# Optimization experiments

Hardware: AMD Instinct MI355X
Metric: run time of the kernel (lower is better)

## Reference

```python
import jax, jax.numpy as jnp
import numpy as np

N, LC, LQ, D = 16, 2048, 256, 256  # D = 2 * LSTM_HIDDEN_DIM


def setup_inputs() -> dict:
    key = jax.random.key(0)
    k1, k2, k3 = jax.random.split(key, 3)
    emb_context = jax.random.normal(k1, (N, LC, D), dtype=jnp.float32)
    emb_query = jax.random.normal(k2, (N, LQ, D), dtype=jnp.float32)
    # Linear(6H=3D, 1, bias=False) weight, flattened to (3D,)
    W = jax.random.normal(k3, (3 * D,), dtype=jnp.float32) / np.sqrt(3 * D)
    return {"emb_context": emb_context, "emb_query": emb_query, "W": W}


def reference(emb_context, emb_query, W):
    d = emb_context.shape[-1]
    # Algebraic decomposition of the expand+cat+linear similarity score:
    # S[n,i,j] = c_i . w_c + q_j . w_q + sum_d c_i[d]*q_j[d]*w_m[d]
    w_c, w_q, w_m = W[:d], W[d:2 * d], W[2 * d:]
    S = (
        jnp.einsum('ncd,d->nc', emb_context, w_c)[:, :, None]
        + jnp.einsum('nqd,d->nq', emb_query, w_q)[:, None, :]
        + jnp.einsum('ncd,nqd->ncq', emb_context * w_m, emb_query)
    )  # (N, Lc, Lq)
    # context-to-query attention
    c2q_attn = jnp.einsum('ncq,nqd->ncd', jax.nn.softmax(S, axis=-1), emb_query)
    # query-to-context attention (max over query dim, softmax over context dim)
    b = jax.nn.softmax(jnp.max(S, axis=2), axis=-1)  # (N, Lc)
    q2c_attn = jnp.einsum('nc,ncd->nd', b, emb_context)[:, None, :]  # (N, 1, D), broadcasts over Lc
    G = jnp.concatenate(
        [emb_context, c2q_attn, emb_context * c2q_attn, emb_context * q2c_attn],
        axis=2,
    )  # (N, Lc, 4D) == (N, Lc, 8*LSTM_HIDDEN_DIM)
    return G
```

## Files before the change

kernel.cpp:

```cpp
#include <hip/hip_runtime.h>
#include <math.h>

#define BN 16
#define LC 2048
#define LQ 256
#define DD 256
#define BM 128
#define NT 512

typedef _Float16 half8 __attribute__((ext_vector_type(8)));
typedef float f32x16 __attribute__((ext_vector_type(16)));

typedef const __attribute__((address_space(1))) void* gas_p;
typedef __attribute__((address_space(3))) void* lds_p;
#define GLOAD_LDS16(gp, lp) \
    __builtin_amdgcn_global_load_lds((gas_p)(gp), (lds_p)(lp), 16, 0, 0)

__device__ __forceinline__ float waveReduceSum(float v) {
#pragma unroll
    for (int o = 32; o > 0; o >>= 1) v += __shfl_xor(v, o, 64);
    return v;
}
__device__ __forceinline__ float waveReduceMax(float v) {
#pragma unroll
    for (int o = 32; o > 0; o >>= 1) v = fmaxf(v, __shfl_xor(v, o, 64));
    return v;
}

__global__ __launch_bounds__(256) void k_prep(const float* __restrict__ q,
                                              const float* __restrict__ W,
                                              _Float16* __restrict__ Qh,
                                              _Float16* __restrict__ QTh,
                                              float* __restrict__ cq) {
    __shared__ float tile[32][257];
    const int n = blockIdx.y;
    const int q0 = blockIdx.x * 32;
    const int t = threadIdx.x;

#pragma unroll
    for (int i = 0; i < 32; ++i) {
        const float v = q[((size_t)(n * LQ + q0 + i)) * DD + t];
        Qh[((size_t)(n * LQ + q0 + i)) * DD + t] = (_Float16)v;
        tile[i][t] = v;
    }
    __syncthreads();

    {
        const int row = t >> 3, sub = t & 7;
        float s = 0.f;
#pragma unroll
        for (int j = 0; j < 32; ++j)
            s = fmaf(tile[row][sub * 32 + j], W[DD + sub * 32 + j], s);
        s += __shfl_xor(s, 1, 64);
        s += __shfl_xor(s, 2, 64);
        s += __shfl_xor(s, 4, 64);
        if (sub == 0) cq[n * LQ + q0 + row] = s;
    }

    const int tx = t & 31, ty = t >> 5;
#pragma unroll
    for (int db = 0; db < 8; ++db) {
#pragma unroll
        for (int i = 0; i < 4; ++i) {
            const int d = db * 32 + ty + 8 * i;
            QTh[((size_t)(n * DD + d)) * LQ + q0 + tx] = (_Float16)tile[tx][d];
        }
    }
}

__global__ __launch_bounds__(NT) void k_main(const float* __restrict__ ctx,
                                             const _Float16* __restrict__ Qh,
                                             const _Float16* __restrict__ QTh,
                                             const float* __restrict__ cq,
                                             const float* __restrict__ W,
                                             float* __restrict__ out,
                                             float* __restrict__ pq,
                                             float* __restrict__ KS) {
    __shared__ _Float16 Abuf[BM * 256];
    __shared__ _Float16 Bbuf[2][256 * 64];
    __shared__ float rowterm[BM];
    __shared__ float eexp[BM];
    __shared__ float redmax[4][BM];
    __shared__ float redsum[4][BM];

    const int t = threadIdx.x;
    const int lane = t & 63, wid = t >> 6;
    const int l31 = lane & 31, lh = lane >> 5;
    const int wr = wid >> 2, wc = wid & 3;
    const int blk = blockIdx.x;
    const int n = blk >> 4;
    const int blk16 = blk & 15;
    const int c0 = blk16 * BM;

    const _Float16* Qhn = Qh + (size_t)n * LQ * DD;
    const _Float16* QThn = QTh + (size_t)n * DD * LQ;

    auto stageB = [&](int kc, const _Float16* src, int buf) {
#pragma unroll
        for (int j = 0; j < 4; ++j) {
            const int r = wid * 32 + j * 8 + (lane >> 3);
            const int gs = (lane & 7) ^ (r & 7);
            const _Float16* gp = src + (size_t)r * 256 + kc * 64 + gs * 8;
            _Float16* lp = &Bbuf[buf][(wid * 32 + j * 8) * 64];
            GLOAD_LDS16(gp, lp);
        }
    };

    auto gemmChunk = [&](f32x16 (&acc)[2][2], int kcA, int buf) {
#pragma unroll
        for (int kk = 0; kk < 4; ++kk) {
            half8 af[2], bf[2];
#pragma unroll
            for (int mt = 0; mt < 2; ++mt) {
                const int row = 64 * wr + 32 * mt + l31;
                const int kb = kcA * 128 + 32 * kk + 16 * lh;
                af[mt] = *(const half8*)((const char*)Abuf + row * 512 + (kb ^ ((row & 7) << 4)));
            }
#pragma unroll
            for (int nt = 0; nt < 2; ++nt) {
                const int row = 64 * wc + 32 * nt + l31;
                const int kb = 32 * kk + 16 * lh;
                bf[nt] = *(const half8*)((const char*)Bbuf[buf] + row * 128 + (kb ^ ((row & 7) << 4)));
            }
#pragma unroll
            for (int mt = 0; mt < 2; ++mt)
#pragma unroll
                for (int nt = 0; nt < 2; ++nt)
                    acc[mt][nt] = __builtin_amdgcn_mfma_f32_32x32x16_f16(af[mt], bf[nt], acc[mt][nt], 0, 0, 0);
        }
    };

    stageB(0, Qhn, 0);

    {
        const int g = t & 31;
        const int r0 = t >> 5;
        float wmv[8], wcv[8];
#pragma unroll
        for (int j = 0; j < 8; ++j) {
            wmv[j] = W[2 * DD + g * 8 + j];
            wcv[j] = W[g * 8 + j];
        }
#pragma unroll
        for (int i = 0; i < 8; ++i) {
            const int r = r0 + 16 * i;
            const size_t gc = (size_t)(n * LC + c0 + r);
            const float* srcr = ctx + gc * DD + g * 8;
            const float4 aa = *(const float4*)srcr;
            const float4 bb = *(const float4*)(srcr + 4);
            float* dstr = out + gc * 1024 + g * 8;
            *(float4*)dstr = aa;
            *(float4*)(dstr + 4) = bb;
            const float vals[8] = {aa.x, aa.y, aa.z, aa.w, bb.x, bb.y, bb.z, bb.w};
            half8 cmv;
            float rt = 0.f;
#pragma unroll
            for (int j = 0; j < 8; ++j) {
                cmv[j] = (_Float16)(vals[j] * wmv[j]);
                rt = fmaf(vals[j], wcv[j], rt);
            }
            *(half8*)((char*)Abuf + r * 512 + ((g * 16) ^ ((r & 7) << 4))) = cmv;
#pragma unroll
            for (int o = 16; o > 0; o >>= 1) rt += __shfl_xor(rt, o, 64);
            if (g == 0) rowterm[r] = rt;
        }
    }
    __syncthreads();

    f32x16 acc[2][2] = {};
#pragma unroll
    for (int kc = 0; kc < 4; ++kc) {
        if (kc) __syncthreads();
        if (kc < 3) stageB(kc + 1, Qhn, (kc + 1) & 1);
        else stageB(0, QThn, 0);
        gemmChunk(acc, kc, kc & 1);
    }
    __syncthreads();

    float cqv[2];
    cqv[0] = cq[n * LQ + 64 * wc + l31];
    cqv[1] = cq[n * LQ + 64 * wc + 32 + l31];

#pragma unroll
    for (int mt = 0; mt < 2; ++mt) {
#pragma unroll
        for (int r = 0; r < 16; ++r) {
            const int rl = 64 * wr + 32 * mt + (r & 3) + 8 * (r >> 2) + 4 * lh;
            const float rterm = rowterm[rl];
            const float v0 = acc[mt][0][r] + rterm + cqv[0];
            const float v1 = acc[mt][1][r] + rterm + cqv[1];
            acc[mt][0][r] = v0;
            acc[mt][1][r] = v1;
            float mx = fmaxf(v0, v1);
#pragma unroll
            for (int o = 16; o > 0; o >>= 1) mx = fmaxf(mx, __shfl_xor(mx, o, 64));
            if (l31 == 0) redmax[wc][rl] = mx;
        }
    }
    __syncthreads();

    if (t < BM) {
        const float mv = fmaxf(fmaxf(redmax[0][t], redmax[1][t]),
                               fmaxf(redmax[2][t], redmax[3][t]));
        const float kb = waveReduceMax(mv);
        const float e = __expf(mv - kb);
        eexp[t] = e;
        const float sb = waveReduceSum(e);
        if (lane == 0) {
            KS[(n * 32 + blk16 * 2 + (t >> 6)) * 2 + 0] = kb;
            KS[(n * 32 + blk16 * 2 + (t >> 6)) * 2 + 1] = sb;
        }
    }

#pragma unroll
    for (int mt = 0; mt < 2; ++mt) {
#pragma unroll
        for (int r = 0; r < 16; ++r) {
            const int rl = 64 * wr + 32 * mt + (r & 3) + 8 * (r >> 2) + 4 * lh;
            const float mrow = fmaxf(fmaxf(redmax[0][rl], redmax[1][rl]),
                                     fmaxf(redmax[2][rl], redmax[3][rl]));
            const float p0 = __expf(acc[mt][0][r] - mrow);
            const float p1 = __expf(acc[mt][1][r] - mrow);
            const int q0 = 64 * wc + l31, q1 = q0 + 32;
            *((_Float16*)((char*)Abuf + rl * 512 + ((q0 * 2) ^ ((rl & 7) << 4)))) = (_Float16)p0;
            *((_Float16*)((char*)Abuf + rl * 512 + ((q1 * 2) ^ ((rl & 7) << 4)))) = (_Float16)p1;
            float sm = p0 + p1;
#pragma unroll
            for (int o = 16; o > 0; o >>= 1) sm += __shfl_xor(sm, o, 64);
            if (l31 == 0) redsum[wc][rl] = sm;
        }
    }
    __syncthreads();

    f32x16 acc2[2][2] = {};
#pragma unroll
    for (int kc = 0; kc < 4; ++kc) {
        if (kc) __syncthreads();
        if (kc < 3) stageB(kc + 1, QThn, (kc + 1) & 1);
        gemmChunk(acc2, kc, kc & 1);
    }

    float pqa[2] = {0.f, 0.f};
#pragma unroll
    for (int mt = 0; mt < 2; ++mt) {
#pragma unroll
        for (int r = 0; r < 16; ++r) {
            const int rl = 64 * wr + 32 * mt + (r & 3) + 8 * (r >> 2) + 4 * lh;
            const float li = 1.0f / (redsum[0][rl] + redsum[1][rl] +
                                     redsum[2][rl] + redsum[3][rl]);
            const float er = eexp[rl];
            const size_t gc = (size_t)(n * LC + c0 + rl);
#pragma unroll
            for (int nt = 0; nt < 2; ++nt) {
                const int col = 64 * wc + 32 * nt + l31;
                const float cv = ctx[gc * DD + col];
                const float ov = acc2[mt][nt][r] * li;
                const size_t ob = gc * 1024 + col;
                out[ob + 256] = ov;
                out[ob + 512] = cv * ov;
                pqa[nt] = fmaf(er, cv, pqa[nt]);
            }
        }
    }
#pragma unroll
    for (int nt = 0; nt < 2; ++nt) {
        pqa[nt] += __shfl_xor(pqa[nt], 32, 64);
        if (lh == 0) {
            const int col = 64 * wc + 32 * nt + l31;
            pq[((size_t)(n * 32 + blk16 * 2 + wr)) * 256 + col] = pqa[nt];
        }
    }
}

__global__ __launch_bounds__(256) void k_tail(const float* __restrict__ ctx,
                                              const float* __restrict__ pq,
                                              const float* __restrict__ KS,
                                              float* __restrict__ out) {
    const int blk = blockIdx.x;
    const int n = blk >> 5;
    const int c0 = (blk & 31) * 64;
    const int t = threadIdx.x;
    const int cg = t & 63;
    const int rs = t >> 6;

    float bmax = -1e30f;
#pragma unroll
    for (int b = 0; b < 32; ++b) bmax = fmaxf(bmax, KS[(n * 32 + b) * 2]);
    float Z = 0.f;
    float4 a = {0.f, 0.f, 0.f, 0.f};
#pragma unroll
    for (int b = 0; b < 32; ++b) {
        const float w = __expf(KS[(n * 32 + b) * 2] - bmax);
        Z = fmaf(w, KS[(n * 32 + b) * 2 + 1], Z);
        const float4 p4 = *(const float4*)&pq[((size_t)(n * 32 + b)) * 256 + cg * 4];
        a.x = fmaf(w, p4.x, a.x);
        a.y = fmaf(w, p4.y, a.y);
        a.z = fmaf(w, p4.z, a.z);
        a.w = fmaf(w, p4.w, a.w);
    }
    const float zi = 1.0f / Z;
    const float4 q2c4 = {a.x * zi, a.y * zi, a.z * zi, a.w * zi};

#pragma unroll
    for (int r = 0; r < 16; ++r) {
        const size_t gc = (size_t)(n * LC + c0 + rs * 16 + r);
        const float4 cv = *(const float4*)&ctx[gc * DD + cg * 4];
        float4 ov;
        ov.x = cv.x * q2c4.x;
        ov.y = cv.y * q2c4.y;
        ov.z = cv.z * q2c4.z;
        ov.w = cv.w * q2c4.w;
        *(float4*)&out[gc * 1024 + 768 + cg * 4] = ov;
    }
}

extern "C" void kernel_launch(void* const* d_in, const int* in_sizes, int n_in,
                              void* d_out, int out_size, void* d_ws, size_t ws_size,
                              hipStream_t stream) {
    const float* ctx = (const float*)d_in[0];
    const float* q = (const float*)d_in[1];
    const float* W = (const float*)d_in[2];
    float* out = (float*)d_out;

    _Float16* Qh = (_Float16*)d_ws;
    _Float16* QTh = Qh + (size_t)BN * LQ * DD;
    float* fws = (float*)(QTh + (size_t)BN * DD * LQ);
    float* cq = fws;
    float* pq = cq + BN * LQ;
    float* KS = pq + BN * 32 * 256;

    k_prep<<<dim3(LQ / 32, BN), 256, 0, stream>>>(q, W, Qh, QTh, cq);
    k_main<<<BN * LC / BM, NT, 0, stream>>>(ctx, Qh, QTh, cq, W, out, pq, KS);
    k_tail<<<BN * LC / 64, 256, 0, stream>>>(ctx, pq, KS, out);
}
```

Measured before the change: 72.91 us.

## Read B operands directly from global memory and drop LDS staging of Q

Removes the double-buffered LDS staging of the Q/Q^T tiles (global_load_lds plus per-chunk barriers) and has each wave load its MFMA B fragments straight from global/L2. This also frees 64KB of LDS, which may allow higher occupancy. The copy of the context into the first output slice moves from the prologue to the epilogue, reusing the ctx values already loaded there. The trade-off is uncoalesced, unshared B loads that are repeated across waves, and MFMA issue that now waits on global latency.

```diff
diff --git a/kernel.cpp b/kernel.cpp
--- a/kernel.cpp
+++ b/kernel.cpp
@@ -10,11 +10,6 @@
 
 typedef _Float16 half8 __attribute__((ext_vector_type(8)));
 typedef float f32x16 __attribute__((ext_vector_type(16)));
-
-typedef const __attribute__((address_space(1))) void* gas_p;
-typedef __attribute__((address_space(3))) void* lds_p;
-#define GLOAD_LDS16(gp, lp) \
-    __builtin_amdgcn_global_load_lds((gas_p)(gp), (lds_p)(lp), 16, 0, 0)
 
 __device__ __forceinline__ float waveReduceSum(float v) {
 #pragma unroll
@@ -77,7 +72,6 @@
                                              float* __restrict__ pq,
                                              float* __restrict__ KS) {
     __shared__ _Float16 Abuf[BM * 256];
-    __shared__ _Float16 Bbuf[2][256 * 64];
     __shared__ float rowterm[BM];
     __shared__ float eexp[BM];
     __shared__ float redmax[4][BM];
@@ -95,42 +89,28 @@
     const _Float16* Qhn = Qh + (size_t)n * LQ * DD;
     const _Float16* QThn = QTh + (size_t)n * DD * LQ;
 
-    auto stageB = [&](int kc, const _Float16* src, int buf) {
-#pragma unroll
-        for (int j = 0; j < 4; ++j) {
-            const int r = wid * 32 + j * 8 + (lane >> 3);
-            const int gs = (lane & 7) ^ (r & 7);
-            const _Float16* gp = src + (size_t)r * 256 + kc * 64 + gs * 8;
-            _Float16* lp = &Bbuf[buf][(wid * 32 + j * 8) * 64];
-            GLOAD_LDS16(gp, lp);
-        }
-    };
-
-    auto gemmChunk = [&](f32x16 (&acc)[2][2], int kcA, int buf) {
+    auto gemmChunk = [&](f32x16 (&acc)[2][2], int kc, const _Float16* Bsrc) {
 #pragma unroll
         for (int kk = 0; kk < 4; ++kk) {
             half8 af[2], bf[2];
 #pragma unroll
+            for (int nt = 0; nt < 2; ++nt) {
+                const int qrow = 64 * wc + 32 * nt + l31;
+                bf[nt] = *(const half8*)(Bsrc + (size_t)qrow * 256 + kc * 64 + 16 * kk + 8 * lh);
+            }
+#pragma unroll
             for (int mt = 0; mt < 2; ++mt) {
                 const int row = 64 * wr + 32 * mt + l31;
-                const int kb = kcA * 128 + 32 * kk + 16 * lh;
+                const int kb = kc * 128 + 32 * kk + 16 * lh;
                 af[mt] = *(const half8*)((const char*)Abuf + row * 512 + (kb ^ ((row & 7) << 4)));
             }
 #pragma unroll
-            for (int nt = 0; nt < 2; ++nt) {
-                const int row = 64 * wc + 32 * nt + l31;
-                const int kb = 32 * kk + 16 * lh;
-                bf[nt] = *(const half8*)((const char*)Bbuf[buf] + row * 128 + (kb ^ ((row & 7) << 4)));
-            }
-#pragma unroll
             for (int mt = 0; mt < 2; ++mt)
 #pragma unroll
                 for (int nt = 0; nt < 2; ++nt)
                     acc[mt][nt] = __builtin_amdgcn_mfma_f32_32x32x16_f16(af[mt], bf[nt], acc[mt][nt], 0, 0, 0);
         }
     };
-
-    stageB(0, Qhn, 0);
 
     {
         const int g = t & 31;
@@ -144,13 +124,9 @@
 #pragma unroll
         for (int i = 0; i < 8; ++i) {
             const int r = r0 + 16 * i;
-            const size_t gc = (size_t)(n * LC + c0 + r);
-            const float* srcr = ctx + gc * DD + g * 8;
+            const float* srcr = ctx + ((size_t)(n * LC + c0 + r)) * DD + g * 8;
             const float4 aa = *(const float4*)srcr;
             const float4 bb = *(const float4*)(srcr + 4);
-            float* dstr = out + gc * 1024 + g * 8;
-            *(float4*)dstr = aa;
-            *(float4*)(dstr + 4) = bb;
             const float vals[8] = {aa.x, aa.y, aa.z, aa.w, bb.x, bb.y, bb.z, bb.w};
             half8 cmv;
             float rt = 0.f;
@@ -169,13 +145,7 @@
 
     f32x16 acc[2][2] = {};
 #pragma unroll
-    for (int kc = 0; kc < 4; ++kc) {
-        if (kc) __syncthreads();
-        if (kc < 3) stageB(kc + 1, Qhn, (kc + 1) & 1);
-        else stageB(0, QThn, 0);
-        gemmChunk(acc, kc, kc & 1);
-    }
-    __syncthreads();
+    for (int kc = 0; kc < 4; ++kc) gemmChunk(acc, kc, Qhn);
 
     float cqv[2];
     cqv[0] = cq[n * LQ + 64 * wc + l31];
@@ -234,11 +204,7 @@
 
     f32x16 acc2[2][2] = {};
 #pragma unroll
-    for (int kc = 0; kc < 4; ++kc) {
-        if (kc) __syncthreads();
-        if (kc < 3) stageB(kc + 1, QThn, (kc + 1) & 1);
-        gemmChunk(acc2, kc, kc & 1);
-    }
+    for (int kc = 0; kc < 4; ++kc) gemmChunk(acc2, kc, QThn);
 
     float pqa[2] = {0.f, 0.f};
 #pragma unroll
@@ -256,6 +222,7 @@
                 const float cv = ctx[gc * DD + col];
                 const float ov = acc2[mt][nt][r] * li;
                 const size_t ob = gc * 1024 + col;
+                out[ob] = cv;
                 out[ob + 256] = ov;
                 out[ob + 512] = cv * ov;
                 pqa[nt] = fmaf(er, cv, pqa[nt]);
```

Result: slower. 78.51 us (+7.7%).

## Remap blocks across XCDs, defer context copy to epilogue, precompute row max/inverse sums

Applied to the files above, without the earlier changes.

Block indices in both kernels are remapped so consecutive blocks of one batch land on the same XCD, improving L2 locality for shared Q data. The copy of the context into the first output slice moves from the prologue to the epilogue, where ctx is already re-read, so it is written alongside the other slices. Row max and reciprocal row sums are computed once per row into shared memory instead of being recomputed per lane. The epilogue loop order is swapped (nt outer) and two extra barriers are added.

```diff
diff --git a/kernel.cpp b/kernel.cpp
--- a/kernel.cpp
+++ b/kernel.cpp
@@ -79,6 +79,8 @@
     __shared__ _Float16 Abuf[BM * 256];
     __shared__ _Float16 Bbuf[2][256 * 64];
     __shared__ float rowterm[BM];
+    __shared__ float m_lds[BM];
+    __shared__ float linv_lds[BM];
     __shared__ float eexp[BM];
     __shared__ float redmax[4][BM];
     __shared__ float redsum[4][BM];
@@ -87,7 +89,8 @@
     const int lane = t & 63, wid = t >> 6;
     const int l31 = lane & 31, lh = lane >> 5;
     const int wr = wid >> 2, wc = wid & 3;
-    const int blk = blockIdx.x;
+    const int bx = blockIdx.x;
+    const int blk = (bx & 7) * 32 + (bx >> 3);
     const int n = blk >> 4;
     const int blk16 = blk & 15;
     const int c0 = blk16 * BM;
@@ -144,13 +147,9 @@
 #pragma unroll
         for (int i = 0; i < 8; ++i) {
             const int r = r0 + 16 * i;
-            const size_t gc = (size_t)(n * LC + c0 + r);
-            const float* srcr = ctx + gc * DD + g * 8;
+            const float* srcr = ctx + ((size_t)(n * LC + c0 + r)) * DD + g * 8;
             const float4 aa = *(const float4*)srcr;
             const float4 bb = *(const float4*)(srcr + 4);
-            float* dstr = out + gc * 1024 + g * 8;
-            *(float4*)dstr = aa;
-            *(float4*)(dstr + 4) = bb;
             const float vals[8] = {aa.x, aa.y, aa.z, aa.w, bb.x, bb.y, bb.z, bb.w};
             half8 cmv;
             float rt = 0.f;
@@ -198,10 +197,12 @@
         }
     }
     __syncthreads();
+    if (t < BM)
+        m_lds[t] = fmaxf(fmaxf(redmax[0][t], redmax[1][t]), fmaxf(redmax[2][t], redmax[3][t]));
+    __syncthreads();
 
     if (t < BM) {
-        const float mv = fmaxf(fmaxf(redmax[0][t], redmax[1][t]),
-                               fmaxf(redmax[2][t], redmax[3][t]));
+        const float mv = m_lds[t];
         const float kb = waveReduceMax(mv);
         const float e = __expf(mv - kb);
         eexp[t] = e;
@@ -217,8 +218,7 @@
 #pragma unroll
         for (int r = 0; r < 16; ++r) {
             const int rl = 64 * wr + 32 * mt + (r & 3) + 8 * (r >> 2) + 4 * lh;
-            const float mrow = fmaxf(fmaxf(redmax[0][rl], redmax[1][rl]),
-                                     fmaxf(redmax[2][rl], redmax[3][rl]));
+            const float mrow = m_lds[rl];
             const float p0 = __expf(acc[mt][0][r] - mrow);
             const float p1 = __expf(acc[mt][1][r] - mrow);
             const int q0 = 64 * wc + l31, q1 = q0 + 32;
@@ -231,6 +231,9 @@
         }
     }
     __syncthreads();
+    if (t < BM)
+        linv_lds[t] = 1.0f / (redsum[0][t] + redsum[1][t] + redsum[2][t] + redsum[3][t]);
+    __syncthreads();
 
     f32x16 acc2[2][2] = {};
 #pragma unroll
@@ -244,21 +247,20 @@
 #pragma unroll
     for (int mt = 0; mt < 2; ++mt) {
 #pragma unroll
-        for (int r = 0; r < 16; ++r) {
-            const int rl = 64 * wr + 32 * mt + (r & 3) + 8 * (r >> 2) + 4 * lh;
-            const float li = 1.0f / (redsum[0][rl] + redsum[1][rl] +
-                                     redsum[2][rl] + redsum[3][rl]);
-            const float er = eexp[rl];
-            const size_t gc = (size_t)(n * LC + c0 + rl);
-#pragma unroll
-            for (int nt = 0; nt < 2; ++nt) {
-                const int col = 64 * wc + 32 * nt + l31;
+        for (int nt = 0; nt < 2; ++nt) {
+            const int col = 64 * wc + 32 * nt + l31;
+#pragma unroll
+            for (int r = 0; r < 16; ++r) {
+                const int rl = 64 * wr + 32 * mt + (r & 3) + 8 * (r >> 2) + 4 * lh;
+                const size_t gc = (size_t)(n * LC + c0 + rl);
+                const float li = linv_lds[rl];
                 const float cv = ctx[gc * DD + col];
                 const float ov = acc2[mt][nt][r] * li;
                 const size_t ob = gc * 1024 + col;
+                out[ob] = cv;
                 out[ob + 256] = ov;
                 out[ob + 512] = cv * ov;
-                pqa[nt] = fmaf(er, cv, pqa[nt]);
+                pqa[nt] = fmaf(eexp[rl], cv, pqa[nt]);
             }
         }
     }
@@ -276,7 +278,8 @@
                                               const float* __restrict__ pq,
                                               const float* __restrict__ KS,
                                               float* __restrict__ out) {
-    const int blk = blockIdx.x;
+    const int bx = blockIdx.x;
+    const int blk = (bx & 7) * 64 + (bx >> 3);
     const int n = blk >> 5;
     const int c0 = (blk & 31) * 64;
     const int t = threadIdx.x;
```

New measurement: 71.51 us. About the same (-1.9%).
